# Performance work log

Measured on AMD Instinct MI355X. Metric: run time of the kernel, lower is better.

## Reference

```python
import jax, jax.numpy as jnp
import numpy as np

B, S, E, H = 8, 1024, 768, 12
D = E // H  # per-head dim


def setup_inputs() -> dict:
    key = jax.random.key(0)
    ks = jax.random.split(key, 9)
    glorot = lambda k: jax.random.normal(k, (E, E), jnp.float32) * np.sqrt(2.0 / (E + E))
    return {
        "inputs": jax.random.normal(ks[0], (B, S, E), jnp.float32),
        "Wq": glorot(ks[1]), "bq": jnp.zeros((E,), jnp.float32),
        "Wk": glorot(ks[2]), "bk": jnp.zeros((E,), jnp.float32),
        "Wv": glorot(ks[3]), "bv": jnp.zeros((E,), jnp.float32),
        "Wo": glorot(ks[4]), "bo": jnp.zeros((E,), jnp.float32),
    }


def reference(inputs, Wq, bq, Wk, bk, Wv, bv, Wo, bo):
    b, s, e = inputs.shape
    # QKV projections then split heads: [B,S,E] -> [B,H,S,D]
    def heads(x):
        return x.reshape(b, s, H, D).transpose(0, 2, 1, 3)
    q = heads(inputs @ Wq + bq)
    k = heads(inputs @ Wk + bk)
    v = heads(inputs @ Wv + bv)
    scale = 1.0 / jnp.sqrt(jnp.asarray(D, inputs.dtype))
    scores = jnp.einsum("bhqd,bhkd->bhqk", q, k) * scale
    weights = jax.nn.softmax(scores, axis=-1)  # attn_drop rate 0 -> identity
    attn = jnp.einsum("bhqk,bhkd->bhqd", weights, v)
    concat = attn.transpose(0, 2, 1, 3).reshape(b, s, e)
    out = concat @ Wo + bo  # proj_drop rate 0 -> identity
    return out
```

## Files before the change

kernel.cpp:

```cpp
#include <hip/hip_runtime.h>
#include <math.h>

#define BB 8
#define SS 1024
#define EE 768
#define HH 12
#define DD 64
#define MM (BB*SS)

typedef __attribute__((ext_vector_type(8))) short short8;
typedef __attribute__((ext_vector_type(4))) short short4v;
typedef __attribute__((ext_vector_type(4))) float f32x4;

static __device__ __forceinline__ short f2bf(float x) {
    unsigned u = __float_as_uint(x);
    u += 0x7fffu + ((u >> 16) & 1u);
    return (short)(u >> 16);
}
static __device__ __forceinline__ short f2bf_fast(float x) {
    return (short)((__float_as_uint(x) + 0x8000u) >> 16);
}

static __device__ __forceinline__ void gload_lds16(const void* g, void* l) {
    __builtin_amdgcn_global_load_lds((__attribute__((address_space(1))) void*)g,
                                     (__attribute__((address_space(3))) void*)l,
                                     16, 0, 0);
}

#define BAR __builtin_amdgcn_s_barrier()
#define VMW(n) asm volatile("s_waitcnt vmcnt(" #n ")" ::: "memory")

__global__ __launch_bounds__(256)
void cast_x(const float* __restrict__ src, short* __restrict__ dst) {
    const long i = ((long)blockIdx.x * 256 + threadIdx.x) * 4;
    float4 v = *(const float4*)&src[i];
    short4v o;
    o.x = f2bf(v.x); o.y = f2bf(v.y); o.z = f2bf(v.z); o.w = f2bf(v.w);
    *(short4v*)&dst[i] = o;
}

__global__ __launch_bounds__(256)
void wcast_t(const float* __restrict__ W0, const float* __restrict__ W1,
             const float* __restrict__ W2, const float* __restrict__ W3,
             short* __restrict__ Wt) {
    __shared__ short T[64][72];
    const int z = blockIdx.z;
    const float* sp = (z == 0) ? W0 : (z == 1) ? W1 : (z == 2) ? W2 : W3;
    short* dp = Wt + (long)z * EE * EE;
    const int i0 = blockIdx.y * 64;
    const int j0 = blockIdx.x * 64;
    const int tid = threadIdx.x;
#pragma unroll
    for (int rep = 0; rep < 4; ++rep) {
        const int r = (tid >> 4) + rep * 16;
        const int c = (tid & 15) * 4;
        float4 v = *(const float4*)&sp[(long)(i0 + r) * EE + j0 + c];
        T[c + 0][r] = f2bf(v.x);
        T[c + 1][r] = f2bf(v.y);
        T[c + 2][r] = f2bf(v.z);
        T[c + 3][r] = f2bf(v.w);
    }
    __syncthreads();
#pragma unroll
    for (int rep = 0; rep < 4; ++rep) {
        const int rr = (tid >> 4) + rep * 16;
        const int cc = (tid & 15) * 4;
        short4v o;
        o.x = T[rr][cc + 0]; o.y = T[rr][cc + 1];
        o.z = T[rr][cc + 2]; o.w = T[rr][cc + 3];
        *(short4v*)&dp[(long)(j0 + rr) * EE + i0 + cc] = o;
    }
}

#define GEMM_CORE(Abase, Bbase, row0, col0)                                     \
    f32x4 acc[4][4];                                                            \
    _Pragma("unroll") for (int i = 0; i < 4; ++i)                               \
        _Pragma("unroll") for (int j = 0; j < 4; ++j)                           \
            acc[i][j] = (f32x4){0.f, 0.f, 0.f, 0.f};                            \
    const int rm = (w & 1) * 64, cn = (w >> 1) * 64;                            \
    for (int k0 = 0; k0 < EE; k0 += 64) {                                       \
        __syncthreads();                                                        \
        _Pragma("unroll") for (int i = 0; i < 4; ++i) {                         \
            const int chunk = w * 256 + i * 64 + lane;                          \
            const int r = chunk >> 3;                                          \
            const int cs = (((chunk & 7) ^ (r & 7)) << 3);                      \
            short* ldsA = Al + (w * 256 + i * 64) * 8;                          \
            short* ldsB = Bl + (w * 256 + i * 64) * 8;                          \
            gload_lds16(&Abase[(long)(row0 + r) * EE + k0 + cs], ldsA);         \
            gload_lds16(&Bbase[(long)(col0 + r) * EE + k0 + cs], ldsB);         \
        }                                                                       \
        __syncthreads();                                                        \
        _Pragma("unroll") for (int ks = 0; ks < 2; ++ks) {                      \
            short8 af[4], bf[4];                                                \
            _Pragma("unroll") for (int t = 0; t < 4; ++t)                       \
                af[t] = *(const short8*)&Al[(rm + t * 16 + m) * 64 +            \
                                            (((ks * 4 + quad) ^ (m & 7)) << 3)]; \
            _Pragma("unroll") for (int t = 0; t < 4; ++t)                       \
                bf[t] = *(const short8*)&Bl[(cn + t * 16 + m) * 64 +            \
                                            (((ks * 4 + quad) ^ (m & 7)) << 3)]; \
            _Pragma("unroll") for (int mt = 0; mt < 4; ++mt)                    \
                _Pragma("unroll") for (int nt = 0; nt < 4; ++nt)                \
                    acc[mt][nt] = __builtin_amdgcn_mfma_f32_16x16x32_bf16(      \
                        af[mt], bf[nt], acc[mt][nt], 0, 0, 0);                  \
        }                                                                       \
    }

#define QSCALE 0.1803368801111204f

#define STG1(Ld, Gbase, gr0, k0)                                              \
    do {                                                                      \
        const int r_ = tid >> 3;                                              \
        const int cs_ = ((tid & 7) ^ (r_ & 7)) << 3;                          \
        gload_lds16(&(Gbase)[(long)((gr0) + r_) * EE + (k0) + cs_],           \
                    (Ld) + w * 512);                                          \
    } while (0)

#define QKV_RDA(Ld, mb)                                                       \
    _Pragma("unroll") for (int t = 0; t < 4; ++t)                             \
        _Pragma("unroll") for (int ks = 0; ks < 2; ++ks)                      \
            af[t][ks] = *(const short8*)&(Ld)[(wr * 128 + ((mb) + t) * 16 + m) * 64 + \
                                              (((ks * 4 + quad) ^ (m & 7)) << 3)];

#define QKV_RDB(Ld)                                                           \
    _Pragma("unroll") for (int t = 0; t < 2; ++t)                             \
        _Pragma("unroll") for (int ks = 0; ks < 2; ++ks)                      \
            bf[t][ks] = *(const short8*)&(Ld)[(wc * 32 + t * 16 + m) * 64 +   \
                                              (((ks * 4 + quad) ^ (m & 7)) << 3)];

#define QKV_MF(mb)                                                            \
    __builtin_amdgcn_s_setprio(1);                                            \
    _Pragma("unroll") for (int mq = 0; mq < 4; ++mq)                          \
        _Pragma("unroll") for (int nq = 0; nq < 2; ++nq)                      \
            _Pragma("unroll") for (int ks = 0; ks < 2; ++ks)                  \
                acc[(mb) + mq][nq] = __builtin_amdgcn_mfma_f32_16x16x32_bf16( \
                    af[mq][ks], bf[nq][ks], acc[(mb) + mq][nq], 0, 0, 0);     \
    __builtin_amdgcn_s_setprio(0);

__global__ __launch_bounds__(512, 2)
void gemm_qkv(const short* __restrict__ Xb, const short* __restrict__ Wt,
              const float* __restrict__ bq, const float* __restrict__ bk,
              const float* __restrict__ bv,
              short* __restrict__ Qb, short* __restrict__ Kb,
              short* __restrict__ Vb) {
    __shared__ short SMEM[49152];
    short* const Ae = SMEM;
    short* const Ao = SMEM + 16384;
    short* const Be = SMEM + 32768;
    short* const Bo = SMEM + 40960;

    const int tid = threadIdx.x;
    const int w = tid >> 6;
    const int m = tid & 15, quad = (tid & 63) >> 4;
    const int wr = w >> 2, wc = w & 3;

    const int flat = blockIdx.x + 18 * blockIdx.y;
    const int id   = (flat & 7) * 72 + (flat >> 3);
    const int lcl  = id % 72;
    const int rt   = (id / 72) * 4 + (lcl & 3);
    const int ct   = lcl >> 2;
    const int row0 = rt * 256;
    const int wsel = ct / 6;
    const int col0w = (ct % 6) * 128;
    const short* Wsel = Wt + (long)wsel * EE * EE;
    const float* bias = (wsel == 0) ? bq : (wsel == 1) ? bk : bv;

    f32x4 acc[8][2];
#pragma unroll
    for (int i = 0; i < 8; ++i)
#pragma unroll
        for (int j = 0; j < 2; ++j) acc[i][j] = (f32x4){0.f, 0.f, 0.f, 0.f};

    STG1(Ae + 0,     Xb,   row0 + 0,    0);
    STG1(Ae + 8192,  Xb,   row0 + 128,  0);
    STG1(Be + 0,     Wsel, col0w + 0,   0);
    STG1(Be + 4096,  Wsel, col0w + 64,  0);
    STG1(Ae + 4096,  Xb,   row0 + 64,   0);
    STG1(Ae + 12288, Xb,   row0 + 192,  0);
    STG1(Bo + 0,     Wsel, col0w + 0,   64);
    STG1(Bo + 4096,  Wsel, col0w + 64,  64);
    STG1(Ao + 0,     Xb,   row0 + 0,    64);
    STG1(Ao + 8192,  Xb,   row0 + 128,  64);
    VMW(6);
    BAR;

#pragma unroll 1
    for (int it = 0; it < 6; ++it) {
        const int kO1 = (2 * it + 1) * 64;
        const int t2 = 2 * it + 2, t3 = 2 * it + 3;
        const int kE2 = (t2 < 12 ? t2 : 11) * 64;
        const int kO3 = (t3 < 12 ? t3 : 11) * 64;
        short8 af[4][2], bf[2][2];
        QKV_RDA(Ae, 0);
        QKV_RDB(Be);
        STG1(Ao + 4096,  Xb, row0 + 64,  kO1);
        STG1(Ao + 12288, Xb, row0 + 192, kO1);
        BAR;
        QKV_MF(0);
        VMW(6);
        BAR;
        QKV_RDA(Ae, 4);
        STG1(Be + 0,     Wsel, col0w + 0,  kE2);
        STG1(Be + 4096,  Wsel, col0w + 64, kE2);
        STG1(Ae + 0,     Xb,   row0 + 0,   kE2);
        STG1(Ae + 8192,  Xb,   row0 + 128, kE2);
        BAR;
        QKV_MF(4);
        VMW(6);
        BAR;
        QKV_RDA(Ao, 0);
        QKV_RDB(Bo);
        STG1(Ae + 4096,  Xb, row0 + 64,  kE2);
        STG1(Ae + 12288, Xb, row0 + 192, kE2);
        BAR;
        QKV_MF(0);
        VMW(6);
        BAR;
        QKV_RDA(Ao, 4);
        STG1(Bo + 0,     Wsel, col0w + 0,  kO3);
        STG1(Bo + 4096,  Wsel, col0w + 64, kO3);
        STG1(Ao + 0,     Xb,   row0 + 0,   kO3);
        STG1(Ao + 8192,  Xb,   row0 + 128, kO3);
        BAR;
        QKV_MF(4);
        VMW(6);
        BAR;
    }

    VMW(0);
    __syncthreads();
    const int b = row0 >> 10, s0 = row0 & 1023;
    short* EP = SMEM;

    if (wsel < 2) {
        const float scale = (wsel == 0) ? QSCALE : 1.0f;
        short* QK = (wsel == 0) ? Qb : Kb;
#pragma unroll
        for (int nt = 0; nt < 2; ++nt) {
            const float bvv = bias[col0w + wc * 32 + nt * 16 + m];
#pragma unroll
            for (int mt = 0; mt < 8; ++mt)
#pragma unroll
                for (int r = 0; r < 4; ++r)
                    EP[(wr * 128 + mt * 16 + quad * 4 + r) * 136 + wc * 32 + nt * 16 + m] =
                        f2bf((acc[mt][nt][r] + bvv) * scale);
        }
        __syncthreads();
#pragma unroll
        for (int rep = 0; rep < 8; ++rep) {
            const int chunk = tid + rep * 512;
            const int row = chunk >> 4;
            const int cc = (chunk & 15) * 8;
            const int colg = col0w + cc;
            const int h = colg >> 6, d = colg & 63;
            short8 v = *(const short8*)&EP[row * 136 + cc];
            *(short8*)&QK[((long)(b * HH + h) * SS + s0 + row) * DD + d] = v;
        }
    } else {
#pragma unroll
        for (int nt = 0; nt < 2; ++nt) {
            const float bvv = bias[col0w + wc * 32 + nt * 16 + m];
#pragma unroll
            for (int mt = 0; mt < 8; ++mt) {
                short4v o;
                o.x = f2bf(acc[mt][nt][0] + bvv);
                o.y = f2bf(acc[mt][nt][1] + bvv);
                o.z = f2bf(acc[mt][nt][2] + bvv);
                o.w = f2bf(acc[mt][nt][3] + bvv);
                *(short4v*)&EP[(wc * 32 + nt * 16 + m) * 264 + wr * 128 + mt * 16 + quad * 4] = o;
            }
        }
        __syncthreads();
#pragma unroll
        for (int rep = 0; rep < 8; ++rep) {
            const int chunk = tid + rep * 512;
            const int col = chunk >> 5;
            const int sc8 = (chunk & 31) * 8;
            const int colg = col0w + col;
            const int h = colg >> 6, d = colg & 63;
            short8 v = *(const short8*)&EP[col * 264 + sc8];
            *(short8*)&Vb[((long)(b * HH + h) * DD + d) * SS + s0 + sc8] = v;
        }
    }
}

__global__ __launch_bounds__(256)
void gemm_proj(const short* __restrict__ Cb, const short* __restrict__ WoT,
               const float* __restrict__ bo, float* __restrict__ out) {
    __shared__ short Al[128 * 64];
    __shared__ short Bl[128 * 64];
    const int tid = threadIdx.x, w = tid >> 6, lane = tid & 63;
    const int m = lane & 15, quad = lane >> 4;

    const int flat = blockIdx.x + 6 * blockIdx.y;
    const int id   = (flat & 7) * 48 + (flat >> 3);
    const int xcd  = id / 48;
    const int lcl  = id % 48;
    const int row0 = (xcd * 8 + (lcl & 7)) * 128;
    const int col0 = (lcl >> 3) * 128;

    GEMM_CORE(Cb, WoT, row0, col0)

#pragma unroll
    for (int nt = 0; nt < 4; ++nt) {
        const int colg = col0 + cn + nt * 16 + m;
        const float bvv = bo[colg];
#pragma unroll
        for (int mt = 0; mt < 4; ++mt)
#pragma unroll
            for (int r = 0; r < 4; ++r) {
                const int srow = row0 + rm + mt * 16 + quad * 4 + r;
                out[(long)srow * EE + colg] = acc[mt][nt][r] + bvv;
            }
    }
}

#define ATTN_STAGE(Kdst, Vdst, k0)                                            \
    do {                                                                      \
        _Pragma("unroll") for (int i = 0; i < 2; ++i) {                       \
            const int chunk = w * 128 + i * 64 + l;                           \
            const int r = chunk >> 3;                                         \
            const int cs = ((chunk & 7) ^ (r & 7)) << 3;                      \
            gload_lds16(&Kg[(long)((k0) + r) * DD + cs],                      \
                        (Kdst) + (w * 128 + i * 64) * 8);                     \
            gload_lds16(&Vg[(long)r * SS + (k0) + cs],                        \
                        (Vdst) + (w * 128 + i * 64) * 8);                     \
        }                                                                     \
    } while (0)

#define ATTN_COMPUTE(Kbuf, Vbuf)                                              \
    do {                                                                      \
        f32x4 sc[2][4];                                                       \
        __builtin_amdgcn_s_setprio(1);                                        \
        _Pragma("unroll") for (int nt = 0; nt < 4; ++nt) {                    \
            const short* kb = (Kbuf) + (nt * 16 + m) * 64;                    \
            short8 b0 = *(const short8*)&kb[(quad ^ (m & 7)) << 3];           \
            short8 b1 = *(const short8*)&kb[((4 + quad) ^ (m & 7)) << 3];     \
            _Pragma("unroll") for (int g = 0; g < 2; ++g) {                   \
                f32x4 a = (f32x4){0.f, 0.f, 0.f, 0.f};                        \
                a = __builtin_amdgcn_mfma_f32_16x16x32_bf16(aq[g][0], b0, a, 0, 0, 0); \
                a = __builtin_amdgcn_mfma_f32_16x16x32_bf16(aq[g][1], b1, a, 0, 0, 0); \
                sc[g][nt] = a;                                                \
            }                                                                 \
        }                                                                     \
        __builtin_amdgcn_s_setprio(0);                                        \
        _Pragma("unroll") for (int g = 0; g < 2; ++g)                         \
            _Pragma("unroll") for (int nt = 0; nt < 4; ++nt)                  \
                _Pragma("unroll") for (int r = 0; r < 4; ++r)                 \
                    sc[g][nt][r] = __builtin_amdgcn_exp2f(sc[g][nt][r]);      \
        short* Pw = Pl + w * 32 * 72;                                         \
        _Pragma("unroll") for (int g = 0; g < 2; ++g)                         \
            _Pragma("unroll") for (int nt = 0; nt < 4; ++nt)                  \
                _Pragma("unroll") for (int r = 0; r < 4; ++r)                 \
                    Pw[(g * 16 + quad * 4 + r) * 72 + nt * 16 + m] =          \
                        f2bf_fast(sc[g][nt][r]);                              \
        short8 ap[2][2];                                                      \
        _Pragma("unroll") for (int g = 0; g < 2; ++g) {                       \
            ap[g][0] = *(const short8*)(Pw + (g * 16 + m) * 72 + quad * 8);   \
            ap[g][1] = *(const short8*)(Pw + (g * 16 + m) * 72 + 32 + quad * 8); \
        }                                                                     \
        __builtin_amdgcn_s_setprio(1);                                        \
        _Pragma("unroll") for (int g = 0; g < 2; ++g) {                       \
            lacc[g] = __builtin_amdgcn_mfma_f32_16x16x32_bf16(ap[g][0], ones, lacc[g], 0, 0, 0); \
            lacc[g] = __builtin_amdgcn_mfma_f32_16x16x32_bf16(ap[g][1], ones, lacc[g], 0, 0, 0); \
        }                                                                     \
        _Pragma("unroll") for (int dt = 0; dt < 4; ++dt) {                    \
            const short* vb = (Vbuf) + (dt * 16 + m) * 64;                    \
            short8 b0 = *(const short8*)&vb[(quad ^ (m & 7)) << 3];           \
            short8 b1 = *(const short8*)&vb[((4 + quad) ^ (m & 7)) << 3];     \
            _Pragma("unroll") for (int g = 0; g < 2; ++g) {                   \
                O[g][dt] = __builtin_amdgcn_mfma_f32_16x16x32_bf16(ap[g][0], b0, O[g][dt], 0, 0, 0); \
                O[g][dt] = __builtin_amdgcn_mfma_f32_16x16x32_bf16(ap[g][1], b1, O[g][dt], 0, 0, 0); \
            }                                                                 \
        }                                                                     \
        __builtin_amdgcn_s_setprio(0);                                        \
    } while (0)

__global__ __launch_bounds__(256)
void attn_mfma(const short* __restrict__ Q,
               const short* __restrict__ K,
               const short* __restrict__ Vt,
               short* __restrict__ out) {
    __shared__ short K0l[64 * 64];
    __shared__ short K1l[64 * 64];
    __shared__ short V0l[64 * 64];
    __shared__ short V1l[64 * 64];
    __shared__ short Pl[4 * 32 * 72];

    const int tid  = threadIdx.x;
    const int w    = tid >> 6;
    const int l    = tid & 63;
    const int m    = l & 15;
    const int quad = l >> 4;

    const int flat = blockIdx.x + 8 * blockIdx.y + 96 * blockIdx.z;
    const int id   = (flat & 7) * 96 + (flat >> 3);
    const int qt   = id & 7;
    const int bh   = id >> 3;
    const int b    = bh / HH;
    const int h    = bh % HH;
    const int q0   = qt * 128;

    const short* Qg = Q  + (long)bh * SS * DD;
    const short* Kg = K  + (long)bh * SS * DD;
    const short* Vg = Vt + (long)bh * DD * SS;

    short8 aq[2][2];
#pragma unroll
    for (int g = 0; g < 2; ++g) {
        const int row = q0 + w * 32 + g * 16 + m;
        aq[g][0] = *(const short8*)(Qg + (long)row * DD + quad * 8);
        aq[g][1] = *(const short8*)(Qg + (long)row * DD + 32 + quad * 8);
    }

    short8 ones;
#pragma unroll
    for (int i = 0; i < 8; ++i) ones[i] = (short)0x3F80;

    f32x4 O[2][4], lacc[2];
#pragma unroll
    for (int g = 0; g < 2; ++g) {
        lacc[g] = (f32x4){0.f, 0.f, 0.f, 0.f};
#pragma unroll
        for (int dt = 0; dt < 4; ++dt) O[g][dt] = (f32x4){0.f, 0.f, 0.f, 0.f};
    }

    ATTN_STAGE(K0l, V0l, 0);
    __syncthreads();

#pragma unroll 1
    for (int kt2 = 0; kt2 < 8; ++kt2) {
        const int k0 = kt2 * 128;
        ATTN_STAGE(K1l, V1l, k0 + 64);
        ATTN_COMPUTE(K0l, V0l);
        __syncthreads();
        if (kt2 < 7) ATTN_STAGE(K0l, V0l, k0 + 128);
        ATTN_COMPUTE(K1l, V1l);
        __syncthreads();
    }

#pragma unroll
    for (int g = 0; g < 2; ++g)
#pragma unroll
        for (int r = 0; r < 4; ++r) {
            const float inv = 1.0f / lacc[g][r];
            const int qo = q0 + w * 32 + g * 16 + quad * 4 + r;
            short* orow = out + ((long)(b * SS + qo)) * EE + h * DD;
#pragma unroll
            for (int dt = 0; dt < 4; ++dt)
                orow[dt * 16 + m] = f2bf(O[g][dt][r] * inv);
        }
}

extern "C" void kernel_launch(void* const* d_in, const int* in_sizes, int n_in,
                              void* d_out, int out_size, void* d_ws, size_t ws_size,
                              hipStream_t stream) {
    const float* X  = (const float*)d_in[0];
    const float* Wq = (const float*)d_in[1];
    const float* bq = (const float*)d_in[2];
    const float* Wk = (const float*)d_in[3];
    const float* bk = (const float*)d_in[4];
    const float* Wv = (const float*)d_in[5];
    const float* bv = (const float*)d_in[6];
    const float* Wo = (const float*)d_in[7];
    const float* bo = (const float*)d_in[8];

    const long SEG = (long)BB * HH * SS * DD;
    const long WSEG = (long)EE * EE;
    short* Xb = (short*)d_ws;
    short* Wt = Xb + SEG;
    short* Qb = Wt + 4 * WSEG;
    short* Kb = Qb + SEG;
    short* Vb = Kb + SEG;
    short* Cb = Vb + SEG;

    cast_x<<<dim3(MM * EE / 4 / 256), 256, 0, stream>>>(X, Xb);
    wcast_t<<<dim3(12, 12, 4), 256, 0, stream>>>(Wq, Wk, Wv, Wo, Wt);

    gemm_qkv<<<dim3(18, 32), 512, 0, stream>>>(Xb, Wt, bq, bk, bv, Qb, Kb, Vb);

    attn_mfma<<<dim3(SS / 128, HH, BB), 256, 0, stream>>>(Qb, Kb, Vb, Cb);

    gemm_proj<<<dim3(6, 64), 256, 0, stream>>>(Cb, Wt + 3 * WSEG, bo,
                                               (float*)d_out);
}
```

Before: 200.6 us.

## Keep softmax probabilities in registers by computing transposed scores

The QK^T MFMA swaps its operands so the score tile comes out transposed, which lets each lane pack its exp'd scores straight into the bf16 A-operand for the PV MFMA with v_cvt_pk_bf16_f32. This removes the LDS round trip for P: the shared-memory buffer, the scalar stores, and the vector reloads. The V operand loads are rearranged into permuted 4-element reads so the key index order matches the new register layout of P. The risk is that the two narrower LDS reads per operand cost more than before, and that a mismatch in the key permutation would silently give wrong results.

```diff
diff --git a/kernel.cpp b/kernel.cpp
--- a/kernel.cpp
+++ b/kernel.cpp
@@ -11,6 +11,7 @@
 typedef __attribute__((ext_vector_type(8))) short short8;
 typedef __attribute__((ext_vector_type(4))) short short4v;
 typedef __attribute__((ext_vector_type(4))) float f32x4;
+typedef __attribute__((ext_vector_type(4))) int int4v;
 
 static __device__ __forceinline__ short f2bf(float x) {
     unsigned u = __float_as_uint(x);
@@ -19,6 +20,15 @@
 }
 static __device__ __forceinline__ short f2bf_fast(float x) {
     return (short)((__float_as_uint(x) + 0x8000u) >> 16);
+}
+
+static __device__ __forceinline__ int cvtpk_bf16(float lo, float hi) {
+    int r;
+    asm("v_cvt_pk_bf16_f32 %0, %1, %2" : "=v"(r) : "v"(lo), "v"(hi));
+    return r;
+}
+static __device__ __forceinline__ short8 i4_to_s8(int4v v) {
+    union { int4v i; short8 s; } u; u.i = v; return u.s;
 }
 
 static __device__ __forceinline__ void gload_lds16(const void* g, void* l) {
@@ -333,12 +343,12 @@
         __builtin_amdgcn_s_setprio(1);                                        \
         _Pragma("unroll") for (int nt = 0; nt < 4; ++nt) {                    \
             const short* kb = (Kbuf) + (nt * 16 + m) * 64;                    \
-            short8 b0 = *(const short8*)&kb[(quad ^ (m & 7)) << 3];           \
-            short8 b1 = *(const short8*)&kb[((4 + quad) ^ (m & 7)) << 3];     \
+            short8 a0 = *(const short8*)&kb[(quad ^ (m & 7)) << 3];           \
+            short8 a1 = *(const short8*)&kb[((4 + quad) ^ (m & 7)) << 3];     \
             _Pragma("unroll") for (int g = 0; g < 2; ++g) {                   \
                 f32x4 a = (f32x4){0.f, 0.f, 0.f, 0.f};                        \
-                a = __builtin_amdgcn_mfma_f32_16x16x32_bf16(aq[g][0], b0, a, 0, 0, 0); \
-                a = __builtin_amdgcn_mfma_f32_16x16x32_bf16(aq[g][1], b1, a, 0, 0, 0); \
+                a = __builtin_amdgcn_mfma_f32_16x16x32_bf16(a0, aq[g][0], a, 0, 0, 0); \
+                a = __builtin_amdgcn_mfma_f32_16x16x32_bf16(a1, aq[g][1], a, 0, 0, 0); \
                 sc[g][nt] = a;                                                \
             }                                                                 \
         }                                                                     \
@@ -347,26 +357,30 @@
             _Pragma("unroll") for (int nt = 0; nt < 4; ++nt)                  \
                 _Pragma("unroll") for (int r = 0; r < 4; ++r)                 \
                     sc[g][nt][r] = __builtin_amdgcn_exp2f(sc[g][nt][r]);      \
-        short* Pw = Pl + w * 32 * 72;                                         \
+        short8 ap[2][2];                                                      \
         _Pragma("unroll") for (int g = 0; g < 2; ++g)                         \
-            _Pragma("unroll") for (int nt = 0; nt < 4; ++nt)                  \
-                _Pragma("unroll") for (int r = 0; r < 4; ++r)                 \
-                    Pw[(g * 16 + quad * 4 + r) * 72 + nt * 16 + m] =          \
-                        f2bf_fast(sc[g][nt][r]);                              \
-        short8 ap[2][2];                                                      \
-        _Pragma("unroll") for (int g = 0; g < 2; ++g) {                       \
-            ap[g][0] = *(const short8*)(Pw + (g * 16 + m) * 72 + quad * 8);   \
-            ap[g][1] = *(const short8*)(Pw + (g * 16 + m) * 72 + 32 + quad * 8); \
-        }                                                                     \
+            _Pragma("unroll") for (int hf = 0; hf < 2; ++hf) {                \
+                int4v wv;                                                     \
+                wv.x = cvtpk_bf16(sc[g][2 * hf + 0][0], sc[g][2 * hf + 0][1]); \
+                wv.y = cvtpk_bf16(sc[g][2 * hf + 0][2], sc[g][2 * hf + 0][3]); \
+                wv.z = cvtpk_bf16(sc[g][2 * hf + 1][0], sc[g][2 * hf + 1][1]); \
+                wv.w = cvtpk_bf16(sc[g][2 * hf + 1][2], sc[g][2 * hf + 1][3]); \
+                ap[g][hf] = i4_to_s8(wv);                                     \
+            }                                                                 \
         __builtin_amdgcn_s_setprio(1);                                        \
         _Pragma("unroll") for (int g = 0; g < 2; ++g) {                       \
             lacc[g] = __builtin_amdgcn_mfma_f32_16x16x32_bf16(ap[g][0], ones, lacc[g], 0, 0, 0); \
             lacc[g] = __builtin_amdgcn_mfma_f32_16x16x32_bf16(ap[g][1], ones, lacc[g], 0, 0, 0); \
         }                                                                     \
+        const int rsw = m & 7, hb = (quad & 1) * 4;                           \
         _Pragma("unroll") for (int dt = 0; dt < 4; ++dt) {                    \
             const short* vb = (Vbuf) + (dt * 16 + m) * 64;                    \
-            short8 b0 = *(const short8*)&vb[(quad ^ (m & 7)) << 3];           \
-            short8 b1 = *(const short8*)&vb[((4 + quad) ^ (m & 7)) << 3];     \
+            short4v l0 = *(const short4v*)&vb[((((quad >> 1) + 0) ^ rsw) << 3) + hb]; \
+            short4v h0 = *(const short4v*)&vb[((((quad >> 1) + 2) ^ rsw) << 3) + hb]; \
+            short4v l1 = *(const short4v*)&vb[((((quad >> 1) + 4) ^ rsw) << 3) + hb]; \
+            short4v h1 = *(const short4v*)&vb[((((quad >> 1) + 6) ^ rsw) << 3) + hb]; \
+            short8 b0 = __builtin_shufflevector(l0, h0, 0, 1, 2, 3, 4, 5, 6, 7); \
+            short8 b1 = __builtin_shufflevector(l1, h1, 0, 1, 2, 3, 4, 5, 6, 7); \
             _Pragma("unroll") for (int g = 0; g < 2; ++g) {                   \
                 O[g][dt] = __builtin_amdgcn_mfma_f32_16x16x32_bf16(ap[g][0], b0, O[g][dt], 0, 0, 0); \
                 O[g][dt] = __builtin_amdgcn_mfma_f32_16x16x32_bf16(ap[g][1], b1, O[g][dt], 0, 0, 0); \
@@ -384,7 +398,6 @@
     __shared__ short K1l[64 * 64];
     __shared__ short V0l[64 * 64];
     __shared__ short V1l[64 * 64];
-    __shared__ short Pl[4 * 32 * 72];
 
     const int tid  = threadIdx.x;
     const int w    = tid >> 6;
```

New measurement: 197.7 us. About the same (-1.4%).
